# Optimization experiments

Hardware: AMD Instinct MI355X
Metric: run time of the kernel (lower is better)

Reference implementation:

```python
import jax, jax.numpy as jnp
import numpy as np

D_MODEL = 1024
N_HEADS = 16


def setup_inputs() -> dict:
    key = jax.random.key(0)
    ks = jax.random.split(key, 7)
    s = 0.02
    x = jax.random.normal(ks[0], (4, 2048, D_MODEL), dtype=jnp.float32)
    Wq = jax.random.normal(ks[1], (D_MODEL, D_MODEL), dtype=jnp.float32) * s
    Wk = jax.random.normal(ks[2], (D_MODEL, D_MODEL), dtype=jnp.float32) * s
    Wv = jax.random.normal(ks[3], (D_MODEL, D_MODEL), dtype=jnp.float32) * s
    bq = jax.random.normal(ks[4], (D_MODEL,), dtype=jnp.float32) * s
    bk = jax.random.normal(ks[5], (D_MODEL,), dtype=jnp.float32) * s
    bv = jax.random.normal(ks[6], (D_MODEL,), dtype=jnp.float32) * s
    return {"x": x, "Wq": Wq, "bq": bq, "Wk": Wk, "bk": bk, "Wv": Wv, "bv": bv}


def reference(x, Wq, bq, Wk, bk, Wv, bv):
    B, S, D = x.shape
    H = N_HEADS
    hd = D // H
    # torch Linear: y = x @ W.T + b
    q = (x @ Wq.T + bq).reshape(B, S, H, hd).transpose(0, 2, 1, 3)  # [B,H,S,hd]
    k = (x @ Wk.T + bk).reshape(B, S, H, hd).transpose(0, 2, 1, 3)
    v = (x @ Wv.T + bv).reshape(B, S, H, hd).transpose(0, 2, 1, 3)
    # NOTE: source scales by sqrt(d_model), not sqrt(head_dim)
    scores = jnp.einsum('bhqd,bhkd->bhqk', q, k) / jnp.sqrt(jnp.float32(D))
    attn = jax.nn.softmax(scores, axis=-1)
    out = jnp.einsum('bhqk,bhkd->bhqd', attn, v)  # [B,H,S,hd]
    return out.transpose(0, 2, 1, 3).reshape(B, S, D)
```

## Files before the change

### kernel.cpp

```cpp
#include <hip/hip_runtime.h>
#include <hip/hip_bf16.h>

#define D_MODEL 1024
#define NHEADS  16
#define HD      64
#define BATCH   4
#define SEQ     2048

#define XELEMS (BATCH * SEQ * D_MODEL)
#define WELEMS (D_MODEL * D_MODEL)

typedef __attribute__((ext_vector_type(8))) short v8s;
typedef __attribute__((ext_vector_type(4))) float v4f;

using bf16 = __hip_bfloat16;

#define GLD_LDS(gp, lp) \
    __builtin_amdgcn_global_load_lds((const __attribute__((address_space(1))) void*)(gp), \
                                     (__attribute__((address_space(3))) void*)(lp), 16, 0, 0)

#if __has_builtin(__builtin_amdgcn_exp2f)
#define EXP2(x) __builtin_amdgcn_exp2f(x)
#else
#define EXP2(x) exp2f(x)
#endif

__device__ __forceinline__ unsigned int f2bf(float f) {
    union { float f; unsigned int u; } c; c.f = f;
    unsigned int u = c.u;
    u += 0x7fffu + ((u >> 16) & 1u);
    return u >> 16;
}

__device__ __forceinline__ unsigned int pack_bf16_hu(float lo, float hi) {
    unsigned int a = __float_as_uint(lo) + 0x8000u;
    unsigned int b = __float_as_uint(hi) + 0x8000u;
    return __builtin_amdgcn_perm(b, a, 0x07060302u);
}

__device__ __forceinline__ unsigned int cvtpk_bf16(float lo, float hi) {
    unsigned int r;
    asm("v_cvt_pk_bf16_f32 %0, %1, %2" : "=v"(r) : "v"(lo), "v"(hi));
    return r;
}

__device__ __forceinline__ uint4 cvt8(const float* p) {
    float4 f0 = ((const float4*)p)[0];
    float4 f1 = ((const float4*)p)[1];
    uint4 r;
    r.x = f2bf(f0.x) | (f2bf(f0.y) << 16);
    r.y = f2bf(f0.z) | (f2bf(f0.w) << 16);
    r.z = f2bf(f1.x) | (f2bf(f1.y) << 16);
    r.w = f2bf(f1.z) | (f2bf(f1.w) << 16);
    return r;
}

__device__ __forceinline__ int detect_isbf(const unsigned short* x16, int tid) {
    unsigned short v = x16[2 * (tid & 63)];
    int e = (v >> 7) & 0xff;
    bool plaus = (e >= 90) && (e <= 141);
    unsigned long long m = __ballot(plaus);
    return (__popcll(m) >= 48) ? 1 : 0;
}

__device__ __forceinline__ void qswap32(unsigned int &a, unsigned int &b) {
#if __has_builtin(__builtin_amdgcn_permlane32_swap)
    auto r = __builtin_amdgcn_permlane32_swap(a, b, false, false);
    a = (unsigned int)r[0]; b = (unsigned int)r[1];
#else
    unsigned int ax = (unsigned int)__shfl_xor((int)a, 32, 64);
    unsigned int bx = (unsigned int)__shfl_xor((int)b, 32, 64);
    if (threadIdx.x & 32) { a = bx; } else { b = ax; }
#endif
}
__device__ __forceinline__ void qswap16(unsigned int &a, unsigned int &b) {
#if __has_builtin(__builtin_amdgcn_permlane16_swap)
    auto r = __builtin_amdgcn_permlane16_swap(a, b, false, false);
    a = (unsigned int)r[0]; b = (unsigned int)r[1];
#else
    unsigned int ax = (unsigned int)__shfl_xor((int)a, 16, 64);
    unsigned int bx = (unsigned int)__shfl_xor((int)b, 16, 64);
    if (threadIdx.x & 16) { a = bx; } else { b = ax; }
#endif
}

__global__ __launch_bounds__(256) void convert_inputs(
    const void* __restrict__ x,
    const void* __restrict__ wq, const void* __restrict__ wk,
    const void* __restrict__ wv,
    const void* __restrict__ bq, const void* __restrict__ bk,
    const void* __restrict__ bv,
    bf16* __restrict__ xbf, bf16* __restrict__ wbf, bf16* __restrict__ bbf)
{
    const int isbf = detect_isbf((const unsigned short*)x, threadIdx.x);
    long g = (long)blockIdx.x * 256 + threadIdx.x;
    const long xg = XELEMS / 8;
    const long wg = WELEMS / 8;
    const long bg = D_MODEL / 8;
    const void* src; bf16* dst; long off;
    if      (g < xg)                  { src = x;  dst = xbf;              off = g; }
    else if (g < xg + wg)             { src = wq; dst = wbf;              off = g - xg; }
    else if (g < xg + 2*wg)           { src = wk; dst = wbf + WELEMS;     off = g - xg - wg; }
    else if (g < xg + 3*wg)           { src = wv; dst = wbf + 2*WELEMS;   off = g - xg - 2*wg; }
    else if (g < xg + 3*wg + bg)      { src = bq; dst = bbf;              off = g - xg - 3*wg; }
    else if (g < xg + 3*wg + 2*bg)    { src = bk; dst = bbf + D_MODEL;    off = g - xg - 3*wg - bg; }
    else if (g < xg + 3*wg + 3*bg)    { src = bv; dst = bbf + 2*D_MODEL;  off = g - xg - 3*wg - 2*bg; }
    else return;
    uint4 r = isbf ? ((const uint4*)src)[off]
                   : cvt8((const float*)src + off * 8);
    ((uint4*)dst)[off] = r;
}

__global__ __launch_bounds__(256, 3) void qkv_gemm(
    const bf16* __restrict__ xbf, const bf16* __restrict__ wbf,
    const bf16* __restrict__ bbf,
    bf16* __restrict__ qout, bf16* __restrict__ kout, bf16* __restrict__ vout)
{
    __shared__ bf16 Atile[2][8 * 512];
    __shared__ bf16 Btile[2][8 * 512];

    const int z = blockIdx.z;
    const bf16* W    = wbf + (size_t)z * WELEMS;
    const bf16* bias = bbf + z * D_MODEL;
    bf16* out = (z == 0) ? qout : (z == 1) ? kout : vout;
    const float scale = (z == 0) ? (1.4426950408889634f / 32.0f) : 1.0f;

    const int tid  = threadIdx.x;
    const int lane = tid & 63;
    const int wave = tid >> 6;
    const int m0w  = (wave >> 1) * 64;
    const int n0w  = (wave & 1) * 64;
    const int m_base = blockIdx.x * 128;
    const int n_base = blockIdx.y * 128;

    const int lm   = lane & 15;
    const int quad = lane >> 4;

    const int slm = lane >> 2;
    const int sq  = lane & 3;
    const int fidx = (lm * 4 + quad) * 8;

    v4f acc[4][4] = {};

    auto stage = [&](int bi, int k0_) {
        #pragma unroll
        for (int j = 0; j < 2; ++j) {
            int rt = wave * 2 + j;
            const bf16* ga = xbf + (size_t)(m_base + rt * 16 + slm) * D_MODEL
                                 + k0_ + sq * 8;
            const bf16* gb = W   + (size_t)(n_base + rt * 16 + slm) * D_MODEL
                                 + k0_ + sq * 8;
            GLD_LDS(ga, &Atile[bi][rt * 512]);
            GLD_LDS(gb, &Btile[bi][rt * 512]);
        }
    };

    stage(0, 0);
    __syncthreads();

    const int NKT = D_MODEL / 32;
    for (int t = 0; t < NKT; ++t) {
        const int cur = t & 1;
        if (t + 1 < NKT) stage(cur ^ 1, (t + 1) * 32);

        v8s af[4], bf[4];
        #pragma unroll
        for (int mt = 0; mt < 4; ++mt)
            af[mt] = *(const v8s*)(&Atile[cur][((m0w >> 4) + mt) * 512] + fidx);
        #pragma unroll
        for (int nt = 0; nt < 4; ++nt)
            bf[nt] = *(const v8s*)(&Btile[cur][((n0w >> 4) + nt) * 512] + fidx);
        #pragma unroll
        for (int mt = 0; mt < 4; ++mt)
            #pragma unroll
            for (int nt = 0; nt < 4; ++nt)
                acc[mt][nt] = __builtin_amdgcn_mfma_f32_16x16x32_bf16(
                    af[mt], bf[nt], acc[mt][nt], 0, 0, 0);

        __syncthreads();
    }

    #pragma unroll
    for (int nt = 0; nt < 4; ++nt) {
        int n = n_base + n0w + nt * 16 + lm;
        float bb = __bfloat162float(bias[n]);
        int h = n >> 6, d = n & 63;
        #pragma unroll
        for (int mt = 0; mt < 4; ++mt) {
            if (z == 2) {
                int m = m_base + m0w + mt * 16 + quad * 4;
                int b = m >> 11, s = m & (SEQ - 1);
                float p0 = acc[mt][nt][0] + bb;
                float p1 = acc[mt][nt][1] + bb;
                float p2 = acc[mt][nt][2] + bb;
                float p3 = acc[mt][nt][3] + bb;
                uint2 pk;
                pk.x = pack_bf16_hu(p0, p1);
                pk.y = pack_bf16_hu(p2, p3);
                size_t bh = (size_t)(b * NHEADS + h);
                *(uint2*)(out + (((bh << 6) + d) << 11) + s) = pk;
            } else {
                #pragma unroll
                for (int r = 0; r < 4; ++r) {
                    int m = m_base + m0w + mt * 16 + quad * 4 + r;
                    int b = m >> 11, s = m & (SEQ - 1);
                    float vv = (acc[mt][nt][r] + bb) * scale;
                    size_t bh = (size_t)(b * NHEADS + h);
                    out[(((bh << 11) + s) << 6) + d] = __float2bfloat16(vv);
                }
            }
        }
    }
}

__global__ __launch_bounds__(256, 4) void attn(
    const bf16* __restrict__ q, const bf16* __restrict__ k,
    const bf16* __restrict__ vT, void* __restrict__ out,
    const unsigned short* __restrict__ x16)
{
    __shared__ bf16 Ks[2][8 * 512];
    __shared__ bf16 Vt[2][8 * 512];

    const int isbf = detect_isbf(x16, threadIdx.x);

    const int l   = blockIdx.x;
    const int idx = l >> 3;
    const int q0  = (idx & 15) * 128;
    const int bh  = (l & 7) + ((idx >> 4) << 3);
    const int b   = bh >> 4, h = bh & 15;
    const size_t head_base  = (size_t)bh * SEQ * HD;
    const size_t head_baseT = (size_t)bh * HD * SEQ;

    const int tid  = threadIdx.x;
    const int lane = tid & 63;
    const int wave = tid >> 6;
    const int lm   = lane & 15;
    const int quad = lane >> 4;

    const int slm = lane >> 2;
    const int sq  = lane & 3;
    const int fidx = (lm * 4 + quad) * 8;

    v8s aq[2][2];
    #pragma unroll
    for (int mt = 0; mt < 2; ++mt)
        #pragma unroll
        for (int kb = 0; kb < 2; ++kb)
            aq[mt][kb] = *(const v8s*)(q + head_base
                          + (size_t)(q0 + wave * 32 + mt * 16 + lm) * HD
                          + kb * 32 + quad * 8);

    float l_acc[2] = { 0.0f, 0.0f };
    v4f   O[2][4] = {};

    typedef union { v8s v; unsigned int u[4]; } AB;

    auto stage = [&](int bi, int kv0_) {
        #pragma unroll
        for (int j = 0; j < 2; ++j) {
            int c  = wave * 2 + j;
            int kt = c >> 1, kb = c & 1;
            const bf16* ga = k + head_base
                + (size_t)(kv0_ + kt * 16 + slm) * HD + kb * 32 + sq * 8;
            GLD_LDS(ga, &Ks[bi][c * 512]);
        }
        #pragma unroll
        for (int j = 0; j < 2; ++j) {
            int c  = wave * 2 + j;
            int g1 = c >> 2, dt = c & 3;
            const bf16* gv = vT + head_baseT
                + (size_t)(dt * 16 + slm) * SEQ + kv0_ + sq * 16 + g1 * 8;
            GLD_LDS(gv, &Vt[bi][c * 512]);
        }
    };

    stage(0, 0);
    __syncthreads();

    const int NT = SEQ / 64;
    for (int t = 0; t < NT; ++t) {
        const int cur = t & 1;
        if (t + 1 < NT) stage(cur ^ 1, (t + 1) * 64);

        v4f sc[4][2] = {};
        #pragma unroll
        for (int kb = 0; kb < 2; ++kb) {
            v8s kf[4];
            #pragma unroll
            for (int kt = 0; kt < 4; ++kt)
                kf[kt] = *(const v8s*)(&Ks[cur][(kt * 2 + kb) * 512] + fidx);
            #pragma unroll
            for (int kt = 0; kt < 4; ++kt)
                #pragma unroll
                for (int mt = 0; mt < 2; ++mt)
                    sc[kt][mt] = __builtin_amdgcn_mfma_f32_16x16x32_bf16(
                        kf[kt], aq[mt][kb], sc[kt][mt], 0, 0, 0);
        }

        unsigned int pw[2][4][2];
        #pragma unroll
        for (int mt = 0; mt < 2; ++mt) {
            #pragma unroll
            for (int kt = 0; kt < 4; ++kt) {
                float p0 = EXP2(sc[kt][mt][0]);
                float p1 = EXP2(sc[kt][mt][1]);
                float p2 = EXP2(sc[kt][mt][2]);
                float p3 = EXP2(sc[kt][mt][3]);
                l_acc[mt] += (p0 + p1) + (p2 + p3);
                pw[mt][kt][0] = cvtpk_bf16(p0, p1);
                pw[mt][kt][1] = cvtpk_bf16(p2, p3);
            }
        }

        #pragma unroll
        for (int mt = 0; mt < 2; ++mt)
            #pragma unroll
            for (int kt0 = 0; kt0 < 2; ++kt0)
                #pragma unroll
                for (int j = 0; j < 2; ++j)
                    qswap32(pw[mt][kt0][j], pw[mt][kt0 + 2][j]);
        #pragma unroll
        for (int mt = 0; mt < 2; ++mt)
            #pragma unroll
            for (int g1 = 0; g1 < 2; ++g1)
                #pragma unroll
                for (int j = 0; j < 2; ++j)
                    qswap16(pw[mt][2 * g1][j], pw[mt][2 * g1 + 1][j]);

        #pragma unroll
        for (int kk = 0; kk < 2; ++kk) {
            v8s bv8[4];
            #pragma unroll
            for (int dt = 0; dt < 4; ++dt)
                bv8[dt] = *(const v8s*)(&Vt[cur][(kk * 4 + dt) * 512] + fidx);
            #pragma unroll
            for (int mt = 0; mt < 2; ++mt) {
                AB a;
                a.u[0] = pw[mt][2 * kk + 0][0];
                a.u[1] = pw[mt][2 * kk + 0][1];
                a.u[2] = pw[mt][2 * kk + 1][0];
                a.u[3] = pw[mt][2 * kk + 1][1];
                #pragma unroll
                for (int dt = 0; dt < 4; ++dt)
                    O[mt][dt] = __builtin_amdgcn_mfma_f32_16x16x32_bf16(
                        a.v, bv8[dt], O[mt][dt], 0, 0, 0);
            }
        }

        __syncthreads();
    }

    float inv[2];
    #pragma unroll
    for (int mt = 0; mt < 2; ++mt) {
        float lsum = l_acc[mt];
        lsum += __shfl_xor(lsum, 16, 64);
        lsum += __shfl_xor(lsum, 32, 64);
        inv[mt] = 1.0f / lsum;
    }

    #pragma unroll
    for (int mt = 0; mt < 2; ++mt) {
        #pragma unroll
        for (int r = 0; r < 4; ++r) {
            float ir = __shfl(inv[mt], quad * 4 + r, 64);
            int s = q0 + wave * 32 + mt * 16 + quad * 4 + r;
            #pragma unroll
            for (int dt = 0; dt < 4; ++dt) {
                int d = dt * 16 + lm;
                size_t off = (size_t)(b * SEQ + s) * D_MODEL + h * HD + d;
                float val = O[mt][dt][r] * ir;
                if (isbf) ((bf16*)out)[off] = __float2bfloat16(val);
                else      ((float*)out)[off] = val;
            }
        }
    }
}

extern "C" void kernel_launch(void* const* d_in, const int* in_sizes, int n_in,
                              void* d_out, int out_size, void* d_ws, size_t ws_size,
                              hipStream_t stream) {
    const void* x  = d_in[0];
    const void* Wq = d_in[1];
    const void* bq = d_in[2];
    const void* Wk = d_in[3];
    const void* bk = d_in[4];
    const void* Wv = d_in[5];
    const void* bv = d_in[6];

    char* ws = (char*)d_ws;
    bf16* wbf  = (bf16*)(ws + 256);
    bf16* bbf  = (bf16*)(ws + 256 + 3 * (size_t)WELEMS * 2);
    bf16* qws  = (bf16*)(ws + 256 + 3 * (size_t)WELEMS * 2 + 8192);
    const size_t per = (size_t)BATCH * NHEADS * SEQ * HD;
    bf16* kws = qws + per;
    bf16* vws = kws + per;

    bf16* xbf = (bf16*)d_out;

    const long ngroups = (long)XELEMS / 8 + 3L * (WELEMS / 8) + 3L * (D_MODEL / 8);
    convert_inputs<<<(int)((ngroups + 255) / 256), 256, 0, stream>>>(
        x, Wq, Wk, Wv, bq, bk, bv, xbf, wbf, bbf);

    dim3 g1(64, 8, 3);
    qkv_gemm<<<g1, 256, 0, stream>>>(xbf, wbf, bbf, qws, kws, vws);

    attn<<<1024, 256, 0, stream>>>(qws, kws, vws, d_out,
                                   (const unsigned short*)x);
}
```

Measured before the change: 240.0 us.

## Replace double-buffered K32 pipeline with single-buffered K64 tiles in QKV GEMM

```diff
diff --git a/kernel.cpp b/kernel.cpp
--- a/kernel.cpp
+++ b/kernel.cpp
@@ -116,8 +116,8 @@
     const bf16* __restrict__ bbf,
     bf16* __restrict__ qout, bf16* __restrict__ kout, bf16* __restrict__ vout)
 {
-    __shared__ bf16 Atile[2][8 * 512];
-    __shared__ bf16 Btile[2][8 * 512];
+    __shared__ bf16 Atile[16 * 512];
+    __shared__ bf16 Btile[16 * 512];
 
     const int z = blockIdx.z;
     const bf16* W    = wbf + (size_t)z * WELEMS;
@@ -142,42 +142,37 @@
 
     v4f acc[4][4] = {};
 
-    auto stage = [&](int bi, int k0_) {
-        #pragma unroll
-        for (int j = 0; j < 2; ++j) {
-            int rt = wave * 2 + j;
+    for (int k0 = 0; k0 < D_MODEL; k0 += 64) {
+        __syncthreads();
+        #pragma unroll
+        for (int j = 0; j < 4; ++j) {
+            int c  = wave * 4 + j;
+            int rt = c >> 1, kb = c & 1;
             const bf16* ga = xbf + (size_t)(m_base + rt * 16 + slm) * D_MODEL
-                                 + k0_ + sq * 8;
+                                 + k0 + kb * 32 + sq * 8;
             const bf16* gb = W   + (size_t)(n_base + rt * 16 + slm) * D_MODEL
-                                 + k0_ + sq * 8;
-            GLD_LDS(ga, &Atile[bi][rt * 512]);
-            GLD_LDS(gb, &Btile[bi][rt * 512]);
-        }
-    };
-
-    stage(0, 0);
-    __syncthreads();
-
-    const int NKT = D_MODEL / 32;
-    for (int t = 0; t < NKT; ++t) {
-        const int cur = t & 1;
-        if (t + 1 < NKT) stage(cur ^ 1, (t + 1) * 32);
-
-        v8s af[4], bf[4];
-        #pragma unroll
-        for (int mt = 0; mt < 4; ++mt)
-            af[mt] = *(const v8s*)(&Atile[cur][((m0w >> 4) + mt) * 512] + fidx);
-        #pragma unroll
-        for (int nt = 0; nt < 4; ++nt)
-            bf[nt] = *(const v8s*)(&Btile[cur][((n0w >> 4) + nt) * 512] + fidx);
-        #pragma unroll
-        for (int mt = 0; mt < 4; ++mt)
+                                 + k0 + kb * 32 + sq * 8;
+            GLD_LDS(ga, Atile + c * 512);
+            GLD_LDS(gb, Btile + c * 512);
+        }
+        __syncthreads();
+
+        #pragma unroll
+        for (int kb = 0; kb < 2; ++kb) {
+            v8s af[4], bf[4];
+            #pragma unroll
+            for (int mt = 0; mt < 4; ++mt)
+                af[mt] = *(const v8s*)(Atile + (((m0w >> 4) + mt) * 2 + kb) * 512 + fidx);
             #pragma unroll
             for (int nt = 0; nt < 4; ++nt)
-                acc[mt][nt] = __builtin_amdgcn_mfma_f32_16x16x32_bf16(
-                    af[mt], bf[nt], acc[mt][nt], 0, 0, 0);
-
-        __syncthreads();
+                bf[nt] = *(const v8s*)(Btile + (((n0w >> 4) + nt) * 2 + kb) * 512 + fidx);
+            #pragma unroll
+            for (int mt = 0; mt < 4; ++mt)
+                #pragma unroll
+                for (int nt = 0; nt < 4; ++nt)
+                    acc[mt][nt] = __builtin_amdgcn_mfma_f32_16x16x32_bf16(
+                        af[mt], bf[nt], acc[mt][nt], 0, 0, 0);
+        }
     }
 
     #pragma unroll
```

After: 228.5 us (median of 2 runs). 4.8% less time.
